# Performance work log

Measured on AMD Instinct MI355X. Metric: run time of the kernel, lower is better.

The kernel has to match this reference:

```python
import jax, jax.numpy as jnp
import numpy as np

N = 50000      # nodes
E = 800000     # edges (before self-loops)
IN_DIM = 256
HID = 32       # per-head hidden of conv1
OUT = 8        # per-head out of conv2 (mean over heads)
H = 4          # heads


def setup_inputs() -> dict:
    key = jax.random.key(0)
    k = jax.random.split(key, 8)
    x = jax.random.normal(k[0], (N, IN_DIM), dtype=jnp.float32)
    src = jax.random.randint(k[1], (E,), 0, N)
    dst = jax.random.randint(k[2], (E,), 0, N)
    # emulate remove_self_loops: perturb any accidental self-loop
    dst = jnp.where(src == dst, (dst + 1) % N, dst)
    edge_index = jnp.stack([src, dst])
    sc1 = 1.0 / np.sqrt(IN_DIM)
    W1 = jax.random.uniform(k[3], (IN_DIM, H * HID), jnp.float32, -sc1, sc1)
    att1 = jax.random.uniform(k[4], (H, HID), jnp.float32, -0.1, 0.1)
    b1 = jnp.zeros((H * HID,), jnp.float32)
    sc2 = 1.0 / np.sqrt(H * HID)
    W2 = jax.random.uniform(k[5], (H * HID, H * OUT), jnp.float32, -sc2, sc2)
    att2 = jax.random.uniform(k[6], (H, OUT), jnp.float32, -0.1, 0.1)
    b2 = jnp.zeros((OUT,), jnp.float32)
    return {"x": x, "edge_index": edge_index, "W1": W1, "att1": att1,
            "b1": b1, "W2": W2, "att2": att2, "b2": b2}


def _segment_softmax(logits, seg, num_segments):
    # logits: [E, H], seg: [E] destination ids. Every segment is non-empty
    # (self-loops added), so no -inf survives.
    m = jnp.full((num_segments, logits.shape[1]), -jnp.inf, logits.dtype)
    m = m.at[seg].max(logits)
    e = jnp.exp(logits - m[seg])
    z = jax.ops.segment_sum(e, seg, num_segments=num_segments)
    return e / (z[seg] + 1e-16)


def _oodgat_conv(x, W, att, bias, src, dst, concat):
    n = x.shape[0]
    h = (x @ W).reshape(n, att.shape[0], att.shape[1])          # [N, H, C]
    s = jax.nn.sigmoid(jnp.einsum('nhc,hc->nh', h, att))        # [N, H] node scores
    si, sj = s[dst], s[src]                                      # [E, H]
    # OODGAT similarity weight (adjust=True): agree-in-distribution term
    logits = si * sj + (1.0 - si) * (1.0 - sj)
    alpha = _segment_softmax(logits, dst, n)                     # [E, H]
    msg = h[src] * alpha[:, :, None]                             # [E, H, C]
    out = jax.ops.segment_sum(msg, dst, num_segments=n)          # [N, H, C]
    out = out.reshape(n, -1) if concat else out.mean(axis=1)
    return out + bias


def reference(x, edge_index, W1, att1, b1, W2, att2, b2):
    n = x.shape[0]
    loop = jnp.arange(n)
    src = jnp.concatenate([edge_index[0], loop])  # add_self_loops
    dst = jnp.concatenate([edge_index[1], loop])
    # eval mode: dropout (drop_input/drop_prob/drop_edge) are identity
    h = jax.nn.elu(_oodgat_conv(x, W1, att1, b1, src, dst, True))
    return _oodgat_conv(h, W2, att2, b2, src, dst, False)
```

## Files before the change

### kernel.cpp

```cpp
#include <hip/hip_runtime.h>
#include <math.h>


typedef __attribute__((ext_vector_type(8))) short bf16x8;
typedef __attribute__((ext_vector_type(4))) float f32x4;

__device__ inline ushort f2bf(float f) {
    uint u = __float_as_uint(f);
    return (ushort)((u + 0x7fffu + ((u >> 16) & 1u)) >> 16);
}
__device__ inline float bf_lo(uint u) { return __uint_as_float(u << 16); }
__device__ inline float bf_hi(uint u) { return __uint_as_float(u & 0xffff0000u); }


__global__ void count_pos_k(const int* __restrict__ dstA, int E, int ET,
                            int* __restrict__ deg, ushort* __restrict__ epos) {
    int e = blockIdx.x * blockDim.x + threadIdx.x;
    if (e >= ET) return;
    int d = (e < E) ? dstA[e] : (e - E);
    epos[e] = (ushort)atomicAdd(&deg[d], 1);
}

__global__ __launch_bounds__(256) void scan_a_k(const int* __restrict__ deg, int n,
                                                int* __restrict__ rowstart,
                                                int* __restrict__ bsum) {
    __shared__ int ts[256];
    int t = threadIdx.x;
    int idx = blockIdx.x * 1024 + t * 4;
    int4 v = make_int4(0, 0, 0, 0);
    if (idx + 3 < n) {
        v = *(const int4*)(deg + idx);
    } else {
        if (idx < n)     v.x = deg[idx];
        if (idx + 1 < n) v.y = deg[idx + 1];
        if (idx + 2 < n) v.z = deg[idx + 2];
        if (idx + 3 < n) v.w = deg[idx + 3];
    }
    int s = v.x + v.y + v.z + v.w;
    ts[t] = s;
    __syncthreads();
#pragma unroll
    for (int off = 1; off < 256; off <<= 1) {
        int u = (t >= off) ? ts[t - off] : 0;
        __syncthreads();
        ts[t] += u;
        __syncthreads();
    }
    int excl = ts[t] - s;
    int p1 = excl + v.x, p2 = p1 + v.y, p3 = p2 + v.z;
    if (idx < n)     rowstart[idx]     = excl;
    if (idx + 1 < n) rowstart[idx + 1] = p1;
    if (idx + 2 < n) rowstart[idx + 2] = p2;
    if (idx + 3 < n) rowstart[idx + 3] = p3;
    if (t == 255) bsum[blockIdx.x] = ts[255];
}

__global__ __launch_bounds__(256) void scan_b_k(const int* __restrict__ bsum, int nb,
                                                int* __restrict__ boff,
                                                int* __restrict__ totalp) {
    __shared__ int ts[256];
    int t = threadIdx.x;
    int v = (t < nb) ? bsum[t] : 0;
    ts[t] = v;
    __syncthreads();
#pragma unroll
    for (int off = 1; off < 256; off <<= 1) {
        int u = (t >= off) ? ts[t - off] : 0;
        __syncthreads();
        ts[t] += u;
        __syncthreads();
    }
    if (t < nb) boff[t] = ts[t] - v;
    if (t == nb - 1) *totalp = ts[t];
}

__global__ void scan_c_k(int* __restrict__ rowstart, const int* __restrict__ boff,
                         int n) {
    int i = blockIdx.x * blockDim.x + threadIdx.x;
    if (i < n) rowstart[i] += boff[i >> 10];
}

__global__ void scatter_k(const int* __restrict__ srcA, const int* __restrict__ dstA,
                          int E, int ET, const int* __restrict__ rowstart,
                          const ushort* __restrict__ epos,
                          ushort* __restrict__ csrc) {
    int e = blockIdx.x * blockDim.x + threadIdx.x;
    if (e >= ET) return;
    int d, s;
    if (e < E) { d = dstA[e]; s = srcA[e]; } else { d = e - E; s = e - E; }
    csrc[rowstart[d] + epos[e]] = (ushort)s;
}


__global__ void prep_wt_k(const float* __restrict__ W, ushort* __restrict__ Wt) {
    int idx = blockIdx.x * blockDim.x + threadIdx.x;
    if (idx >= 256 * 128) return;
    int k = idx >> 7, col = idx & 127;
    Wt[col * 256 + k] = f2bf(W[idx]);
}


__global__ __launch_bounds__(256) void gemm1_k(const float* __restrict__ X,
                                               const ushort* __restrict__ Wt,
                                               const float* __restrict__ ATT1,
                                               uint* __restrict__ H1b,
                                               float* __restrict__ S1, int n) {
    __shared__ __align__(16) ushort Alds[4][128][8];
    __shared__ __align__(16) ushort Blds[4][128][8];
    __shared__ float att1s[128];
    int tid = threadIdx.x;
    int wid = tid >> 6;
    int lane = tid & 63;
    int g = lane >> 4;
    int lr = lane & 15;
    int brow = blockIdx.x * 128;
    if (tid < 128) att1s[tid] = ATT1[tid];

    f32x4 acc[2][8];
#pragma unroll
    for (int rt = 0; rt < 2; ++rt)
#pragma unroll
        for (int ct = 0; ct < 8; ++ct) acc[rt][ct] = (f32x4){0.f, 0.f, 0.f, 0.f};

    for (int k0 = 0; k0 < 256; k0 += 32) {
#pragma unroll
        for (int rep = 0; rep < 2; ++rep) {
            int idx = tid + rep * 256;
            int r = idx >> 2, koct = idx & 3;
            int gr = brow + r;
            float4 a0, a1;
            if (gr < n) {
                const float* p = X + (size_t)gr * 256 + k0 + koct * 8;
                a0 = *(const float4*)p;
                a1 = *(const float4*)(p + 4);
            } else {
                a0 = a1 = make_float4(0.f, 0.f, 0.f, 0.f);
            }
            uint4 pk;
            pk.x = (uint)f2bf(a0.x) | ((uint)f2bf(a0.y) << 16);
            pk.y = (uint)f2bf(a0.z) | ((uint)f2bf(a0.w) << 16);
            pk.z = (uint)f2bf(a1.x) | ((uint)f2bf(a1.y) << 16);
            pk.w = (uint)f2bf(a1.z) | ((uint)f2bf(a1.w) << 16);
            *(uint4*)&Alds[koct][r][0] = pk;
        }
#pragma unroll
        for (int rep = 0; rep < 2; ++rep) {
            int idx = tid + rep * 256;
            int col = idx & 127, koct = idx >> 7;
            *(uint4*)&Blds[koct][col][0] =
                *(const uint4*)(Wt + (size_t)col * 256 + k0 + koct * 8);
        }
        __syncthreads();
        bf16x8 xf0 = *(bf16x8*)&Alds[g][wid * 32 + lr][0];
        bf16x8 xf1 = *(bf16x8*)&Alds[g][wid * 32 + 16 + lr][0];
#pragma unroll
        for (int ct = 0; ct < 8; ++ct) {
            bf16x8 wf = *(bf16x8*)&Blds[g][ct * 16 + lr][0];
            acc[0][ct] = __builtin_amdgcn_mfma_f32_16x16x32_bf16(wf, xf0, acc[0][ct], 0, 0, 0);
            acc[1][ct] = __builtin_amdgcn_mfma_f32_16x16x32_bf16(wf, xf1, acc[1][ct], 0, 0, 0);
        }
        __syncthreads();
    }
#pragma unroll
    for (int rt = 0; rt < 2; ++rt) {
        int row = brow + wid * 32 + rt * 16 + lr;
        if (row < n) {
#pragma unroll
            for (int ct = 0; ct < 8; ++ct) {
                uint lo = (uint)f2bf(acc[rt][ct][0]) | ((uint)f2bf(acc[rt][ct][1]) << 16);
                uint hi = (uint)f2bf(acc[rt][ct][2]) | ((uint)f2bf(acc[rt][ct][3]) << 16);
                *(uint2*)(H1b + (size_t)row * 64 + ct * 8 + g * 2) = make_uint2(lo, hi);
            }
        }
        float sc[4] = {0.f, 0.f, 0.f, 0.f};
#pragma unroll
        for (int ct = 0; ct < 8; ++ct) {
            int base = ct * 16 + g * 4;
#pragma unroll
            for (int j = 0; j < 4; ++j)
                sc[ct >> 1] = fmaf(acc[rt][ct][j], att1s[base + j], sc[ct >> 1]);
        }
#pragma unroll
        for (int h = 0; h < 4; ++h) {
            sc[h] += __shfl_xor(sc[h], 16);
            sc[h] += __shfl_xor(sc[h], 32);
        }
        if (g == 0 && row < n) {
            float4 sv;
            sv.x = 1.f / (1.f + __expf(-sc[0]));
            sv.y = 1.f / (1.f + __expf(-sc[1]));
            sv.z = 1.f / (1.f + __expf(-sc[2]));
            sv.w = 1.f / (1.f + __expf(-sc[3]));
            *(float4*)(S1 + (size_t)row * 4) = sv;
        }
    }
}


__global__ __launch_bounds__(512) void conv1_k(const uint* __restrict__ H1b,
                                               const float* __restrict__ S1,
                                               const int* __restrict__ rowstart,
                                               const ushort* __restrict__ csrc,
                                               const float* __restrict__ b1,
                                               const float* __restrict__ W2,
                                               const float* __restrict__ ATT2,
                                               ushort* __restrict__ H2b,
                                               float* __restrict__ S2, int n) {
    __shared__ float w2t[32][132];
    __shared__ float rowbuf[8][128];
    __shared__ float wbuf[8][32][4];
    __shared__ ushort srcs[8][32];
    __shared__ float att2s[32];
    int tid = threadIdx.x;
    for (int idx = tid; idx < 4096; idx += 512) {
        int k = idx >> 5, c = idx & 31;
        w2t[c][k] = W2[idx];
    }
    if (tid < 32) att2s[tid] = ATT2[tid];
    __syncthreads();

    int wid = tid >> 6;
    int lane = tid & 63;
    int dst = blockIdx.x * 8 + wid;
    bool valid = dst < n;
    int hd = lane >> 4;
    float4 si4 = valid ? *(const float4*)(S1 + (size_t)dst * 4)
                       : make_float4(0.f, 0.f, 0.f, 0.f);
    int rs = 0, re = 0;
    if (valid) { rs = rowstart[dst]; re = rowstart[dst + 1]; }

    float z0 = 0.f, z1 = 0.f, z2 = 0.f, z3 = 0.f;
    float x0 = 0.f, x1 = 0.f, x2 = 0.f, x3 = 0.f;
    float y0 = 0.f, y1 = 0.f, y2 = 0.f, y3 = 0.f;

    for (int cb = rs; cb < re; cb += 32) {
        int cnt = min(32, re - cb);
        if (lane < cnt) {
            int s = csrc[cb + lane];
            float4 sj = *(const float4*)(S1 + (size_t)s * 4);
            float w0 = __expf(fmaf(si4.x, sj.x, (1.f - si4.x) * (1.f - sj.x)));
            float w1 = __expf(fmaf(si4.y, sj.y, (1.f - si4.y) * (1.f - sj.y)));
            float w2 = __expf(fmaf(si4.z, sj.z, (1.f - si4.z) * (1.f - sj.z)));
            float w3 = __expf(fmaf(si4.w, sj.w, (1.f - si4.w) * (1.f - sj.w)));
            *(float4*)&wbuf[wid][lane][0] = make_float4(w0, w1, w2, w3);
            srcs[wid][lane] = (ushort)s;
        }
        asm volatile("s_waitcnt lgkmcnt(0)" ::: "memory");
        int e = 0;
        for (; e + 3 < cnt; e += 4) {
            int sA = (int)srcs[wid][e];
            int sB = (int)srcs[wid][e + 1];
            int sC = (int)srcs[wid][e + 2];
            int sD = (int)srcs[wid][e + 3];
            sA = __builtin_amdgcn_readfirstlane(sA);
            sB = __builtin_amdgcn_readfirstlane(sB);
            sC = __builtin_amdgcn_readfirstlane(sC);
            sD = __builtin_amdgcn_readfirstlane(sD);
            float wA = wbuf[wid][e][hd];
            float wB = wbuf[wid][e + 1][hd];
            float wC = wbuf[wid][e + 2][hd];
            float wD = wbuf[wid][e + 3][hd];
            uint uA = H1b[(size_t)sA * 64 + lane];
            uint uB = H1b[(size_t)sB * 64 + lane];
            uint uC = H1b[(size_t)sC * 64 + lane];
            uint uD = H1b[(size_t)sD * 64 + lane];
            z0 += wA; z1 += wB; z2 += wC; z3 += wD;
            x0 = fmaf(wA, bf_lo(uA), x0); x1 = fmaf(wB, bf_lo(uB), x1);
            x2 = fmaf(wC, bf_lo(uC), x2); x3 = fmaf(wD, bf_lo(uD), x3);
            y0 = fmaf(wA, bf_hi(uA), y0); y1 = fmaf(wB, bf_hi(uB), y1);
            y2 = fmaf(wC, bf_hi(uC), y2); y3 = fmaf(wD, bf_hi(uD), y3);
        }
        for (; e < cnt; ++e) {
            int s = (int)srcs[wid][e];
            s = __builtin_amdgcn_readfirstlane(s);
            float w = wbuf[wid][e][hd];
            uint u = H1b[(size_t)s * 64 + lane];
            z0 += w;
            x0 = fmaf(w, bf_lo(u), x0);
            y0 = fmaf(w, bf_hi(u), y0);
        }
        asm volatile("" ::: "memory");
    }
    float inv = 1.f / ((z0 + z1) + (z2 + z3) + 1e-16f);
    float r0 = ((x0 + x1) + (x2 + x3)) * inv + b1[lane * 2];
    float r1 = ((y0 + y1) + (y2 + y3)) * inv + b1[lane * 2 + 1];
    r0 = (r0 > 0.f) ? r0 : (__expf(r0) - 1.f);
    r1 = (r1 > 0.f) ? r1 : (__expf(r1) - 1.f);

    *(float2*)&rowbuf[wid][lane * 2] = make_float2(r0, r1);
    int half = lane >> 5, c = lane & 31;
    const float* rb = &rowbuf[wid][half * 64];
    const float* wr = &w2t[c][half * 64];
    float sum = 0.f;
#pragma unroll
    for (int k = 0; k < 64; k += 4) {
        float4 rv = *(const float4*)(rb + k);
        float4 wv = *(const float4*)(wr + k);
        sum = fmaf(rv.x, wv.x, sum);
        sum = fmaf(rv.y, wv.y, sum);
        sum = fmaf(rv.z, wv.z, sum);
        sum = fmaf(rv.w, wv.w, sum);
    }
    sum += __shfl_xor(sum, 32);
    if (valid && half == 0) H2b[(size_t)dst * 32 + c] = f2bf(sum);

    float v = sum * att2s[c];
    v += __shfl_xor(v, 1);
    v += __shfl_xor(v, 2);
    v += __shfl_xor(v, 4);
    if (valid && half == 0 && (c & 7) == 0)
        S2[dst * 4 + (c >> 3)] = 1.f / (1.f + __expf(-v));
}


__global__ __launch_bounds__(256) void conv2_k(const uint* __restrict__ H2u,
                                               const float* __restrict__ S,
                                               const int* __restrict__ rowstart,
                                               const ushort* __restrict__ csrc,
                                               const float* __restrict__ b2,
                                               float* __restrict__ Out, int n) {
    int gtid = blockIdx.x * blockDim.x + threadIdx.x;
    int wave = gtid >> 6;
    int lane = threadIdx.x & 63;
    int q = lane >> 4;
    int c2 = lane & 15;
    int dst = wave * 4 + q;
    if (dst >= n) return;
    int hd = c2 >> 2;
    float si = S[dst * 4 + hd];
    float omsi = 1.f - si;
    int rs = rowstart[dst], re = rowstart[dst + 1];

    float z0 = 0.f, z1 = 0.f, z2 = 0.f, z3 = 0.f;
    float x0 = 0.f, x1 = 0.f, x2 = 0.f, x3 = 0.f;
    float y0 = 0.f, y1 = 0.f, y2 = 0.f, y3 = 0.f;
    int i = rs;
    for (; i + 3 < re; i += 4) {
        int s0 = csrc[i], s1 = csrc[i + 1], s2 = csrc[i + 2], s3 = csrc[i + 3];
        float sj0 = S[s0 * 4 + hd], sj1 = S[s1 * 4 + hd];
        float sj2 = S[s2 * 4 + hd], sj3 = S[s3 * 4 + hd];
        uint u0 = H2u[(size_t)s0 * 16 + c2];
        uint u1 = H2u[(size_t)s1 * 16 + c2];
        uint u2 = H2u[(size_t)s2 * 16 + c2];
        uint u3 = H2u[(size_t)s3 * 16 + c2];
        float w0 = __expf(fmaf(si, sj0, omsi * (1.f - sj0)));
        float w1 = __expf(fmaf(si, sj1, omsi * (1.f - sj1)));
        float w2 = __expf(fmaf(si, sj2, omsi * (1.f - sj2)));
        float w3 = __expf(fmaf(si, sj3, omsi * (1.f - sj3)));
        z0 += w0; z1 += w1; z2 += w2; z3 += w3;
        x0 = fmaf(w0, bf_lo(u0), x0); x1 = fmaf(w1, bf_lo(u1), x1);
        x2 = fmaf(w2, bf_lo(u2), x2); x3 = fmaf(w3, bf_lo(u3), x3);
        y0 = fmaf(w0, bf_hi(u0), y0); y1 = fmaf(w1, bf_hi(u1), y1);
        y2 = fmaf(w2, bf_hi(u2), y2); y3 = fmaf(w3, bf_hi(u3), y3);
    }
    for (; i < re; ++i) {
        int s0 = csrc[i];
        float sj0 = S[s0 * 4 + hd];
        uint u0 = H2u[(size_t)s0 * 16 + c2];
        float w0 = __expf(fmaf(si, sj0, omsi * (1.f - sj0)));
        z0 += w0;
        x0 = fmaf(w0, bf_lo(u0), x0);
        y0 = fmaf(w0, bf_hi(u0), y0);
    }
    float inv = 1.f / (((z0 + z1) + (z2 + z3)) + 1e-16f);
    float r0 = ((x0 + x1) + (x2 + x3)) * inv;
    float r1 = ((y0 + y1) + (y2 + y3)) * inv;
    r0 += __shfl_xor(r0, 4, 16); r0 += __shfl_xor(r0, 8, 16);
    r1 += __shfl_xor(r1, 4, 16); r1 += __shfl_xor(r1, 8, 16);
    if (c2 < 4) {
        float2 o = make_float2(r0 * 0.25f + b2[2 * c2],
                               r1 * 0.25f + b2[2 * c2 + 1]);
        *(float2*)(Out + (size_t)dst * 8 + 2 * c2) = o;
    }
}


static inline size_t align16(size_t x) { return (x + 15) & ~(size_t)15; }

extern "C" void kernel_launch(void* const* d_in, const int* in_sizes, int n_in,
                              void* d_out, int out_size, void* d_ws, size_t ws_size,
                              hipStream_t stream) {
    const float* x    = (const float*)d_in[0];
    const int*   edge = (const int*)d_in[1];
    const float* W1   = (const float*)d_in[2];
    const float* att1 = (const float*)d_in[3];
    const float* b1   = (const float*)d_in[4];
    const float* W2   = (const float*)d_in[5];
    const float* att2 = (const float*)d_in[6];
    const float* b2   = (const float*)d_in[7];

    int N  = in_sizes[0] / 256;
    int E  = in_sizes[1] / 2;
    int ET = E + N;
    int NB = (N + 1023) / 1024;
    const int* srcA = edge;
    const int* dstA = edge + E;

    char* ws = (char*)d_ws;
    uint*  h1b  = (uint*)ws;   ws += align16((size_t)N * 64 * sizeof(uint));
    ushort* h2b = (ushort*)ws; ws += align16((size_t)N * 32 * sizeof(ushort));
    float* s1   = (float*)ws;  ws += align16((size_t)N * 4 * sizeof(float));
    float* s2   = (float*)ws;  ws += align16((size_t)N * 4 * sizeof(float));
    int* rowstart = (int*)ws;  ws += align16((size_t)(N + 1) * sizeof(int));
    int* deg      = (int*)ws;  ws += align16((size_t)N * sizeof(int));
    ushort* csrc  = (ushort*)ws; ws += align16((size_t)ET * sizeof(ushort));
    ushort* epos  = (ushort*)ws; ws += align16((size_t)ET * sizeof(ushort));
    int* bsum     = (int*)ws;  ws += align16((size_t)NB * sizeof(int));
    int* boff     = (int*)ws;  ws += align16((size_t)NB * sizeof(int));
    ushort* w1t   = (ushort*)ws; ws += align16((size_t)256 * 128 * sizeof(ushort));

    hipMemsetAsync(deg, 0, (size_t)N * sizeof(int), stream);

    int eb = (ET + 255) / 256;
    count_pos_k<<<eb, 256, 0, stream>>>(dstA, E, ET, deg, epos);
    scan_a_k<<<NB, 256, 0, stream>>>(deg, N, rowstart, bsum);
    scan_b_k<<<1, 256, 0, stream>>>(bsum, NB, boff, rowstart + N);
    scan_c_k<<<(N + 255) / 256, 256, 0, stream>>>(rowstart, boff, N);
    scatter_k<<<eb, 256, 0, stream>>>(srcA, dstA, E, ET, rowstart, epos, csrc);

    prep_wt_k<<<(256 * 128 + 255) / 256, 256, 0, stream>>>(W1, w1t);
    gemm1_k<<<(N + 127) / 128, 256, 0, stream>>>(x, w1t, att1, h1b, s1, N);
    conv1_k<<<(N + 7) / 8, 512, 0, stream>>>(h1b, s1, rowstart, csrc, b1, W2, att2,
                                             h2b, s2, N);
    int waves2 = (N + 3) / 4;
    conv2_k<<<(waves2 * 64 + 255) / 256, 256, 0, stream>>>((const uint*)h2b, s2,
                                                           rowstart, csrc, b2,
                                                           (float*)d_out, N);
}
```

Measured before the change: 160.7 us.

## Make conv kernels persistent grid-stride with wider edge batching and per-edge lane split

conv1 becomes a persistent grid-stride kernel over destination nodes, loading W2 once per block. It also processes edge chunks of 64 using readlane on register-held sources instead of LDS, with 8-way unrolled gathers. conv2 now assigns one wave per destination node, splitting edges across four lane groups with shuffle reductions, also grid-stride. The aim is more memory-level parallelism and less launch and setup overhead per node, at the cost of extra reductions and fixed grid sizes.

```diff
diff --git a/kernel.cpp b/kernel.cpp
--- a/kernel.cpp
+++ b/kernel.cpp
@@ -197,19 +197,19 @@
 }
 
 
-__global__ __launch_bounds__(512) void conv1_k(const uint* __restrict__ H1b,
-                                               const float* __restrict__ S1,
-                                               const int* __restrict__ rowstart,
-                                               const ushort* __restrict__ csrc,
-                                               const float* __restrict__ b1,
-                                               const float* __restrict__ W2,
-                                               const float* __restrict__ ATT2,
-                                               ushort* __restrict__ H2b,
-                                               float* __restrict__ S2, int n) {
+__global__ __launch_bounds__(512, 8) void conv1_k(const uint* __restrict__ H1b,
+                                                  const float* __restrict__ S1,
+                                                  const int* __restrict__ rowstart,
+                                                  const ushort* __restrict__ csrc,
+                                                  const float* __restrict__ b1,
+                                                  const float* __restrict__ W2,
+                                                  const float* __restrict__ ATT2,
+                                                  ushort* __restrict__ H2b,
+                                                  float* __restrict__ S2,
+                                                  int n, int nwaves) {
     __shared__ float w2t[32][132];
     __shared__ float rowbuf[8][128];
-    __shared__ float wbuf[8][32][4];
-    __shared__ ushort srcs[8][32];
+    __shared__ float wbuf[8][64][4];
     __shared__ float att2s[32];
     int tid = threadIdx.x;
     for (int idx = tid; idx < 4096; idx += 512) {
@@ -221,156 +221,162 @@
 
     int wid = tid >> 6;
     int lane = tid & 63;
-    int dst = blockIdx.x * 8 + wid;
-    bool valid = dst < n;
     int hd = lane >> 4;
-    float4 si4 = valid ? *(const float4*)(S1 + (size_t)dst * 4)
-                       : make_float4(0.f, 0.f, 0.f, 0.f);
-    int rs = 0, re = 0;
-    if (valid) { rs = rowstart[dst]; re = rowstart[dst + 1]; }
-
-    float z0 = 0.f, z1 = 0.f, z2 = 0.f, z3 = 0.f;
-    float x0 = 0.f, x1 = 0.f, x2 = 0.f, x3 = 0.f;
-    float y0 = 0.f, y1 = 0.f, y2 = 0.f, y3 = 0.f;
-
-    for (int cb = rs; cb < re; cb += 32) {
-        int cnt = min(32, re - cb);
-        if (lane < cnt) {
-            int s = csrc[cb + lane];
-            float4 sj = *(const float4*)(S1 + (size_t)s * 4);
-            float w0 = __expf(fmaf(si4.x, sj.x, (1.f - si4.x) * (1.f - sj.x)));
-            float w1 = __expf(fmaf(si4.y, sj.y, (1.f - si4.y) * (1.f - sj.y)));
-            float w2 = __expf(fmaf(si4.z, sj.z, (1.f - si4.z) * (1.f - sj.z)));
-            float w3 = __expf(fmaf(si4.w, sj.w, (1.f - si4.w) * (1.f - sj.w)));
-            *(float4*)&wbuf[wid][lane][0] = make_float4(w0, w1, w2, w3);
-            srcs[wid][lane] = (ushort)s;
-        }
+    int half = lane >> 5, cc2 = lane & 31;
+    int gwave = blockIdx.x * 8 + wid;
+    float2 b1v = *(const float2*)(b1 + lane * 2);
+
+    for (int dst = gwave; dst < n; dst += nwaves) {
+        int rs = rowstart[dst], re = rowstart[dst + 1];
+        float4 si4 = *(const float4*)(S1 + (size_t)dst * 4);
+        float z0 = 0.f, z1 = 0.f, z2 = 0.f, z3 = 0.f;
+        float x0 = 0.f, x1 = 0.f, x2 = 0.f, x3 = 0.f;
+        float y0 = 0.f, y1 = 0.f, y2 = 0.f, y3 = 0.f;
+
+        for (int cb = rs; cb < re; cb += 64) {
+            int cc = min(64, re - cb);
+            int sv = 0;
+            if (lane < cc) {
+                sv = csrc[cb + lane];
+                float4 sj = *(const float4*)(S1 + (size_t)sv * 4);
+                float w0 = __expf(fmaf(si4.x, sj.x, (1.f - si4.x) * (1.f - sj.x)));
+                float w1 = __expf(fmaf(si4.y, sj.y, (1.f - si4.y) * (1.f - sj.y)));
+                float w2 = __expf(fmaf(si4.z, sj.z, (1.f - si4.z) * (1.f - sj.z)));
+                float w3 = __expf(fmaf(si4.w, sj.w, (1.f - si4.w) * (1.f - sj.w)));
+                *(float4*)&wbuf[wid][lane][0] = make_float4(w0, w1, w2, w3);
+            }
+            asm volatile("s_waitcnt lgkmcnt(0)" ::: "memory");
+            int e = 0;
+            for (; e + 7 < cc; e += 8) {
+                int sA = __builtin_amdgcn_readlane(sv, e);
+                int sB = __builtin_amdgcn_readlane(sv, e + 1);
+                int sC = __builtin_amdgcn_readlane(sv, e + 2);
+                int sD = __builtin_amdgcn_readlane(sv, e + 3);
+                int sE = __builtin_amdgcn_readlane(sv, e + 4);
+                int sF = __builtin_amdgcn_readlane(sv, e + 5);
+                int sG = __builtin_amdgcn_readlane(sv, e + 6);
+                int sH = __builtin_amdgcn_readlane(sv, e + 7);
+                float wA = wbuf[wid][e][hd],     wB = wbuf[wid][e + 1][hd];
+                float wC = wbuf[wid][e + 2][hd], wD = wbuf[wid][e + 3][hd];
+                float wE = wbuf[wid][e + 4][hd], wF = wbuf[wid][e + 5][hd];
+                float wG = wbuf[wid][e + 6][hd], wH = wbuf[wid][e + 7][hd];
+                uint uA = H1b[(size_t)sA * 64 + lane];
+                uint uB = H1b[(size_t)sB * 64 + lane];
+                uint uC = H1b[(size_t)sC * 64 + lane];
+                uint uD = H1b[(size_t)sD * 64 + lane];
+                uint uE = H1b[(size_t)sE * 64 + lane];
+                uint uF = H1b[(size_t)sF * 64 + lane];
+                uint uG = H1b[(size_t)sG * 64 + lane];
+                uint uH = H1b[(size_t)sH * 64 + lane];
+                z0 += wA + wE; z1 += wB + wF; z2 += wC + wG; z3 += wD + wH;
+                x0 = fmaf(wA, bf_lo(uA), x0); x1 = fmaf(wB, bf_lo(uB), x1);
+                x2 = fmaf(wC, bf_lo(uC), x2); x3 = fmaf(wD, bf_lo(uD), x3);
+                x0 = fmaf(wE, bf_lo(uE), x0); x1 = fmaf(wF, bf_lo(uF), x1);
+                x2 = fmaf(wG, bf_lo(uG), x2); x3 = fmaf(wH, bf_lo(uH), x3);
+                y0 = fmaf(wA, bf_hi(uA), y0); y1 = fmaf(wB, bf_hi(uB), y1);
+                y2 = fmaf(wC, bf_hi(uC), y2); y3 = fmaf(wD, bf_hi(uD), y3);
+                y0 = fmaf(wE, bf_hi(uE), y0); y1 = fmaf(wF, bf_hi(uF), y1);
+                y2 = fmaf(wG, bf_hi(uG), y2); y3 = fmaf(wH, bf_hi(uH), y3);
+            }
+            for (; e < cc; ++e) {
+                int s = __builtin_amdgcn_readlane(sv, e);
+                float w = wbuf[wid][e][hd];
+                uint u = H1b[(size_t)s * 64 + lane];
+                z0 += w;
+                x0 = fmaf(w, bf_lo(u), x0);
+                y0 = fmaf(w, bf_hi(u), y0);
+            }
+            asm volatile("" ::: "memory");
+        }
+        float inv = 1.f / ((z0 + z1) + (z2 + z3) + 1e-16f);
+        float r0 = ((x0 + x1) + (x2 + x3)) * inv + b1v.x;
+        float r1 = ((y0 + y1) + (y2 + y3)) * inv + b1v.y;
+        r0 = (r0 > 0.f) ? r0 : (__expf(r0) - 1.f);
+        r1 = (r1 > 0.f) ? r1 : (__expf(r1) - 1.f);
+
+        *(float2*)&rowbuf[wid][lane * 2] = make_float2(r0, r1);
         asm volatile("s_waitcnt lgkmcnt(0)" ::: "memory");
-        int e = 0;
-        for (; e + 3 < cnt; e += 4) {
-            int sA = (int)srcs[wid][e];
-            int sB = (int)srcs[wid][e + 1];
-            int sC = (int)srcs[wid][e + 2];
-            int sD = (int)srcs[wid][e + 3];
-            sA = __builtin_amdgcn_readfirstlane(sA);
-            sB = __builtin_amdgcn_readfirstlane(sB);
-            sC = __builtin_amdgcn_readfirstlane(sC);
-            sD = __builtin_amdgcn_readfirstlane(sD);
-            float wA = wbuf[wid][e][hd];
-            float wB = wbuf[wid][e + 1][hd];
-            float wC = wbuf[wid][e + 2][hd];
-            float wD = wbuf[wid][e + 3][hd];
-            uint uA = H1b[(size_t)sA * 64 + lane];
-            uint uB = H1b[(size_t)sB * 64 + lane];
-            uint uC = H1b[(size_t)sC * 64 + lane];
-            uint uD = H1b[(size_t)sD * 64 + lane];
-            z0 += wA; z1 += wB; z2 += wC; z3 += wD;
-            x0 = fmaf(wA, bf_lo(uA), x0); x1 = fmaf(wB, bf_lo(uB), x1);
-            x2 = fmaf(wC, bf_lo(uC), x2); x3 = fmaf(wD, bf_lo(uD), x3);
-            y0 = fmaf(wA, bf_hi(uA), y0); y1 = fmaf(wB, bf_hi(uB), y1);
-            y2 = fmaf(wC, bf_hi(uC), y2); y3 = fmaf(wD, bf_hi(uD), y3);
-        }
-        for (; e < cnt; ++e) {
-            int s = (int)srcs[wid][e];
-            s = __builtin_amdgcn_readfirstlane(s);
-            float w = wbuf[wid][e][hd];
-            uint u = H1b[(size_t)s * 64 + lane];
-            z0 += w;
-            x0 = fmaf(w, bf_lo(u), x0);
-            y0 = fmaf(w, bf_hi(u), y0);
-        }
-        asm volatile("" ::: "memory");
-    }
-    float inv = 1.f / ((z0 + z1) + (z2 + z3) + 1e-16f);
-    float r0 = ((x0 + x1) + (x2 + x3)) * inv + b1[lane * 2];
-    float r1 = ((y0 + y1) + (y2 + y3)) * inv + b1[lane * 2 + 1];
-    r0 = (r0 > 0.f) ? r0 : (__expf(r0) - 1.f);
-    r1 = (r1 > 0.f) ? r1 : (__expf(r1) - 1.f);
-
-    *(float2*)&rowbuf[wid][lane * 2] = make_float2(r0, r1);
-    int half = lane >> 5, c = lane & 31;
-    const float* rb = &rowbuf[wid][half * 64];
-    const float* wr = &w2t[c][half * 64];
-    float sum = 0.f;
-#pragma unroll
-    for (int k = 0; k < 64; k += 4) {
-        float4 rv = *(const float4*)(rb + k);
-        float4 wv = *(const float4*)(wr + k);
-        sum = fmaf(rv.x, wv.x, sum);
-        sum = fmaf(rv.y, wv.y, sum);
-        sum = fmaf(rv.z, wv.z, sum);
-        sum = fmaf(rv.w, wv.w, sum);
-    }
-    sum += __shfl_xor(sum, 32);
-    if (valid && half == 0) H2b[(size_t)dst * 32 + c] = f2bf(sum);
-
-    float v = sum * att2s[c];
-    v += __shfl_xor(v, 1);
-    v += __shfl_xor(v, 2);
-    v += __shfl_xor(v, 4);
-    if (valid && half == 0 && (c & 7) == 0)
-        S2[dst * 4 + (c >> 3)] = 1.f / (1.f + __expf(-v));
-}
-
-
-__global__ __launch_bounds__(256) void conv2_k(const uint* __restrict__ H2u,
-                                               const float* __restrict__ S,
-                                               const int* __restrict__ rowstart,
-                                               const ushort* __restrict__ csrc,
-                                               const float* __restrict__ b2,
-                                               float* __restrict__ Out, int n) {
-    int gtid = blockIdx.x * blockDim.x + threadIdx.x;
-    int wave = gtid >> 6;
+        const float* rb = &rowbuf[wid][half * 64];
+        const float* wr = &w2t[cc2][half * 64];
+        float sum = 0.f;
+#pragma unroll
+        for (int k = 0; k < 64; k += 4) {
+            float4 rv = *(const float4*)(rb + k);
+            float4 wv = *(const float4*)(wr + k);
+            sum = fmaf(rv.x, wv.x, sum);
+            sum = fmaf(rv.y, wv.y, sum);
+            sum = fmaf(rv.z, wv.z, sum);
+            sum = fmaf(rv.w, wv.w, sum);
+        }
+        sum += __shfl_xor(sum, 32);
+        if (half == 0) H2b[(size_t)dst * 32 + cc2] = f2bf(sum);
+
+        float v = sum * att2s[cc2];
+        v += __shfl_xor(v, 1);
+        v += __shfl_xor(v, 2);
+        v += __shfl_xor(v, 4);
+        if (half == 0 && (cc2 & 7) == 0)
+            S2[dst * 4 + (cc2 >> 3)] = 1.f / (1.f + __expf(-v));
+    }
+}
+
+
+__global__ __launch_bounds__(256, 8) void conv2_k(const uint* __restrict__ H2u,
+                                                  const float* __restrict__ S,
+                                                  const int* __restrict__ rowstart,
+                                                  const ushort* __restrict__ csrc,
+                                                  const float* __restrict__ b2,
+                                                  float* __restrict__ Out,
+                                                  int n, int nwaves) {
+    int gwave = (int)((blockIdx.x * blockDim.x + threadIdx.x) >> 6);
     int lane = threadIdx.x & 63;
-    int q = lane >> 4;
+    int eslot = lane >> 4;
     int c2 = lane & 15;
-    int dst = wave * 4 + q;
-    if (dst >= n) return;
     int hd = c2 >> 2;
-    float si = S[dst * 4 + hd];
-    float omsi = 1.f - si;
-    int rs = rowstart[dst], re = rowstart[dst + 1];
-
-    float z0 = 0.f, z1 = 0.f, z2 = 0.f, z3 = 0.f;
-    float x0 = 0.f, x1 = 0.f, x2 = 0.f, x3 = 0.f;
-    float y0 = 0.f, y1 = 0.f, y2 = 0.f, y3 = 0.f;
-    int i = rs;
-    for (; i + 3 < re; i += 4) {
-        int s0 = csrc[i], s1 = csrc[i + 1], s2 = csrc[i + 2], s3 = csrc[i + 3];
-        float sj0 = S[s0 * 4 + hd], sj1 = S[s1 * 4 + hd];
-        float sj2 = S[s2 * 4 + hd], sj3 = S[s3 * 4 + hd];
-        uint u0 = H2u[(size_t)s0 * 16 + c2];
-        uint u1 = H2u[(size_t)s1 * 16 + c2];
-        uint u2 = H2u[(size_t)s2 * 16 + c2];
-        uint u3 = H2u[(size_t)s3 * 16 + c2];
-        float w0 = __expf(fmaf(si, sj0, omsi * (1.f - sj0)));
-        float w1 = __expf(fmaf(si, sj1, omsi * (1.f - sj1)));
-        float w2 = __expf(fmaf(si, sj2, omsi * (1.f - sj2)));
-        float w3 = __expf(fmaf(si, sj3, omsi * (1.f - sj3)));
-        z0 += w0; z1 += w1; z2 += w2; z3 += w3;
-        x0 = fmaf(w0, bf_lo(u0), x0); x1 = fmaf(w1, bf_lo(u1), x1);
-        x2 = fmaf(w2, bf_lo(u2), x2); x3 = fmaf(w3, bf_lo(u3), x3);
-        y0 = fmaf(w0, bf_hi(u0), y0); y1 = fmaf(w1, bf_hi(u1), y1);
-        y2 = fmaf(w2, bf_hi(u2), y2); y3 = fmaf(w3, bf_hi(u3), y3);
-    }
-    for (; i < re; ++i) {
-        int s0 = csrc[i];
-        float sj0 = S[s0 * 4 + hd];
-        uint u0 = H2u[(size_t)s0 * 16 + c2];
-        float w0 = __expf(fmaf(si, sj0, omsi * (1.f - sj0)));
-        z0 += w0;
-        x0 = fmaf(w0, bf_lo(u0), x0);
-        y0 = fmaf(w0, bf_hi(u0), y0);
-    }
-    float inv = 1.f / (((z0 + z1) + (z2 + z3)) + 1e-16f);
-    float r0 = ((x0 + x1) + (x2 + x3)) * inv;
-    float r1 = ((y0 + y1) + (y2 + y3)) * inv;
-    r0 += __shfl_xor(r0, 4, 16); r0 += __shfl_xor(r0, 8, 16);
-    r1 += __shfl_xor(r1, 4, 16); r1 += __shfl_xor(r1, 8, 16);
-    if (c2 < 4) {
-        float2 o = make_float2(r0 * 0.25f + b2[2 * c2],
-                               r1 * 0.25f + b2[2 * c2 + 1]);
-        *(float2*)(Out + (size_t)dst * 8 + 2 * c2) = o;
+    float2 b2v;
+    b2v.x = b2[2 * (c2 & 3)];
+    b2v.y = b2[2 * (c2 & 3) + 1];
+
+    for (int dst = gwave; dst < n; dst += nwaves) {
+        float si = S[dst * 4 + hd];
+        float omsi = 1.f - si;
+        int rs = rowstart[dst], re = rowstart[dst + 1];
+        int cnt = re - rs;
+        float z = 0.f, x = 0.f, y = 0.f;
+        int i = eslot;
+        for (; i + 4 < cnt; i += 8) {
+            int s0 = csrc[rs + i];
+            int s1 = csrc[rs + i + 4];
+            float sj0 = S[s0 * 4 + hd];
+            float sj1 = S[s1 * 4 + hd];
+            uint u0 = H2u[(size_t)s0 * 16 + c2];
+            uint u1 = H2u[(size_t)s1 * 16 + c2];
+            float w0 = __expf(fmaf(si, sj0, omsi * (1.f - sj0)));
+            float w1 = __expf(fmaf(si, sj1, omsi * (1.f - sj1)));
+            z += w0 + w1;
+            x = fmaf(w0, bf_lo(u0), x); x = fmaf(w1, bf_lo(u1), x);
+            y = fmaf(w0, bf_hi(u0), y); y = fmaf(w1, bf_hi(u1), y);
+        }
+        if (i < cnt) {
+            int s0 = csrc[rs + i];
+            float sj0 = S[s0 * 4 + hd];
+            uint u0 = H2u[(size_t)s0 * 16 + c2];
+            float w0 = __expf(fmaf(si, sj0, omsi * (1.f - sj0)));
+            z += w0;
+            x = fmaf(w0, bf_lo(u0), x);
+            y = fmaf(w0, bf_hi(u0), y);
+        }
+        z += __shfl_xor(z, 16); z += __shfl_xor(z, 32);
+        x += __shfl_xor(x, 16); x += __shfl_xor(x, 32);
+        y += __shfl_xor(y, 16); y += __shfl_xor(y, 32);
+        float inv = 1.f / (z + 1e-16f);
+        float r0 = x * inv, r1 = y * inv;
+        r0 += __shfl_xor(r0, 4, 16); r0 += __shfl_xor(r0, 8, 16);
+        r1 += __shfl_xor(r1, 4, 16); r1 += __shfl_xor(r1, 8, 16);
+        if (eslot == 0 && c2 < 4) {
+            float2 o = make_float2(r0 * 0.25f + b2v.x, r1 * 0.25f + b2v.y);
+            *(float2*)(Out + (size_t)dst * 8 + 2 * c2) = o;
+        }
     }
 }
 
@@ -420,10 +426,16 @@
 
     prep_wt_k<<<(256 * 128 + 255) / 256, 256, 0, stream>>>(W1, w1t);
     gemm1_k<<<(N + 127) / 128, 256, 0, stream>>>(x, w1t, att1, h1b, s1, N);
-    conv1_k<<<(N + 7) / 8, 512, 0, stream>>>(h1b, s1, rowstart, csrc, b1, W2, att2,
-                                             h2b, s2, N);
-    int waves2 = (N + 3) / 4;
-    conv2_k<<<(waves2 * 64 + 255) / 256, 256, 0, stream>>>((const uint*)h2b, s2,
-                                                           rowstart, csrc, b2,
-                                                           (float*)d_out, N);
-}
+
+    int c1_blocks = 1024;
+    if (c1_blocks > (N + 7) / 8) c1_blocks = (N + 7) / 8;
+    int c1_waves = c1_blocks * 8;
+    conv1_k<<<c1_blocks, 512, 0, stream>>>(h1b, s1, rowstart, csrc, b1, W2, att2,
+                                           h2b, s2, N, c1_waves);
+
+    int c2_blocks = 2048;
+    if (c2_blocks > (N + 3) / 4) c2_blocks = (N + 3) / 4;
+    int c2_waves = c2_blocks * 4;
+    conv2_k<<<c2_blocks, 256, 0, stream>>>((const uint*)h2b, s2, rowstart, csrc, b2,
+                                           (float*)d_out, N, c2_waves);
+}
```

Result: faster. 154.8 us (-3.7%).
